# Kernel tuning notes

Measured on AMD Instinct MI355X. Metric: run time of the kernel, lower is better.

The kernel has to match this reference:

```python
import jax, jax.numpy as jnp
import numpy as np

B, S, D, H = 2, 2048, 512, 8
E = D // H  # per-head depth = 64


def setup_inputs() -> dict:
    key = jax.random.key(0)
    ks = jax.random.split(key, 10)
    x = jax.random.normal(ks[0], (B, S, D), dtype=jnp.float32)
    # binary mask: 1 = masked position (added as -1e9)
    attention_mask = jax.random.randint(ks[1], (B, S, S), 0, 2, dtype=jnp.int32)
    # per-head Dense weights stacked: [H, D, E] (Keras Dense: y = x @ W + b)
    sc = 1.0 / np.sqrt(D)
    Wq = jax.random.normal(ks[2], (H, D, E), dtype=jnp.float32) * sc
    Wk = jax.random.normal(ks[3], (H, D, E), dtype=jnp.float32) * sc
    Wv = jax.random.normal(ks[4], (H, D, E), dtype=jnp.float32) * sc
    bq = jnp.zeros((H, E), dtype=jnp.float32)
    bk = jnp.zeros((H, E), dtype=jnp.float32)
    bv = jnp.zeros((H, E), dtype=jnp.float32)
    Wo = jax.random.normal(ks[5], (D, D), dtype=jnp.float32) * sc
    bo = jnp.zeros((D,), dtype=jnp.float32)
    return {"x": x, "attention_mask": attention_mask, "Wq": Wq, "bq": bq,
            "Wk": Wk, "bk": bk, "Wv": Wv, "bv": bv, "Wo": Wo, "bo": bo}


def reference(x, attention_mask, Wq, bq, Wk, bk, Wv, bv, Wo, bo):
    # Per-head Dense projections, vectorized over heads: [B,H,S,E]
    q = jnp.einsum('bsd,hde->bhse', x, Wq) + bq[None, :, None, :]
    k = jnp.einsum('bsd,hde->bhse', x, Wk) + bk[None, :, None, :]
    v = jnp.einsum('bsd,hde->bhse', x, Wv) + bv[None, :, None, :]
    # scaled dot-product attention
    scores = jnp.einsum('bhse,bhte->bhst', q, k) / jnp.sqrt(jnp.float32(E))
    scores = scores + (-1e9) * attention_mask.astype(jnp.float32)[:, None, :, :]
    weights = jax.nn.softmax(scores, axis=-1)
    o = jnp.einsum('bhst,bhte->bhse', weights, v)
    # concat heads (head i -> columns [i*E:(i+1)*E]) then output Dense
    o = o.transpose(0, 2, 1, 3).reshape(B, S, D)
    return o @ Wo + bo
```

## Files before the change

### kernel.cpp

```cpp
#include <hip/hip_runtime.h>
#include <hip/hip_bf16.h>

typedef unsigned short u16;
typedef unsigned int u32;
typedef unsigned long long u64;
typedef short s16x8 __attribute__((ext_vector_type(8)));
typedef float f32x4 __attribute__((ext_vector_type(4)));
typedef float f32x16 __attribute__((ext_vector_type(16)));
typedef int i32x4 __attribute__((ext_vector_type(4)));

static __device__ __forceinline__ u16 f2b(float f) {
    union { float f; unsigned u; } x; x.f = f;
    unsigned r = x.u + 0x7fffu + ((x.u >> 16) & 1u);
    return (u16)(r >> 16);
}

static __device__ __forceinline__ u32 pkbf2(float a, float b) {
    union { __hip_bfloat162 h; u32 u; } c;
    c.h = __float22bfloat162_rn(make_float2(a, b));
    return c.u;
}

static __device__ __forceinline__ f32x16 zero16() {
    f32x16 z;
#pragma unroll
    for (int i = 0; i < 16; i++) z[i] = 0.f;
    return z;
}

static __device__ __forceinline__ s16x8 mk8(u32 a, u32 b, u32 c, u32 d) {
    union { u32 u[4]; s16x8 v; } x;
    x.u[0] = a; x.u[1] = b; x.u[2] = c; x.u[3] = d;
    return x.v;
}

static __device__ __forceinline__ u32 sx32(u32 v) {
    return (u32)__shfl_xor((int)v, 32, 64);
}

static __device__ __forceinline__ void gll16(const u16* g, u16* l) {
    __builtin_amdgcn_global_load_lds(
        (const __attribute__((address_space(1))) u32*)g,
        (__attribute__((address_space(3))) u32*)l, 16, 0, 0);
}


__global__ __launch_bounds__(256)
void k_pack_all(const float* __restrict__ x, const int* __restrict__ mask,
                const float* __restrict__ Wq, const float* __restrict__ Wk,
                const float* __restrict__ Wv, const float* __restrict__ Wo,
                const float* __restrict__ bq, const float* __restrict__ bk,
                const float* __restrict__ bv, const float* __restrict__ bo,
                u16* __restrict__ xb, u16* __restrict__ WT, u16* __restrict__ WoT,
                float* __restrict__ bias, u32* __restrict__ mb) {
    int idx = blockIdx.x * 256 + threadIdx.x;
    if (idx < 524288) {
        int i = idx * 4;
        float4 v = *(const float4*)(x + i);
        ushort4 o;
        o.x = f2b(v.x); o.y = f2b(v.y); o.z = f2b(v.z); o.w = f2b(v.w);
        *(ushort4*)(xb + i) = o;
    } else if (idx < 1310720) {
        int t = idx - 524288;
        int z = t >> 18, r = t & 262143;
        const float* W = (z == 0) ? Wq : (z == 1) ? Wk : Wv;
        int n = r >> 9, d = r & 511;
        WT[t] = f2b(W[((n >> 6) * 512 + d) * 64 + (n & 63)]);
    } else if (idx < 1572864) {
        int r = idx - 1310720;
        int n = r >> 9, d = r & 511;
        WoT[r] = f2b(Wo[d * 512 + n]);
    } else if (idx < 1574912) {
        int i = idx - 1572864;
        float v;
        if (i < 512) v = bq[i];
        else if (i < 1024) v = bk[i - 512];
        else if (i < 1536) v = bv[i - 1024];
        else v = bo[i - 1536];
        bias[i] = v;
    } else {
        int i2 = idx - 1574912;
        const int* p = mask + (size_t)i2 * 32;
        unsigned wv2 = 0;
#pragma unroll
        for (int j = 0; j < 32; j += 4) {
            int4 v = *(const int4*)(p + j);
            wv2 |= ((unsigned)(v.x & 1) << j) | ((unsigned)(v.y & 1) << (j + 1)) |
                   ((unsigned)(v.z & 1) << (j + 2)) | ((unsigned)(v.w & 1) << (j + 3));
        }
        mb[i2] = wv2;
    }
}


template<int MF, bool F32OUT>
__global__ __launch_bounds__(256)
void k_gemm(const u16* __restrict__ A, const u16* __restrict__ BTbase,
            const float* __restrict__ biasBase,
            u16* __restrict__ Cb, u16* __restrict__ Vt, float* __restrict__ Cf) {
    const int BM = MF * 32;
    const int nblk = blockIdx.x, mblk = blockIdx.y, z = blockIdx.z;
    const u16* BT = BTbase + (size_t)z * 262144;
    const float* bias = biasBase + z * 512;
    __shared__ __align__(16) u16 As[MF * 32 * 64];
    __shared__ __align__(16) u16 Bs[128 * 64];
    const int tid = threadIdx.x, lane = tid & 63, wv = tid >> 6;
    const int lr = lane & 15, lg = lane >> 4;
    const int wr = (wv >> 1) * (MF * 16), wc = (wv & 1) * 64;
    const u16* Ag = A + (size_t)(mblk * BM) * 512;
    const u16* Bg = BT + (size_t)(nblk * 128) * 512;

    f32x4 acc[MF][4];
#pragma unroll
    for (int i = 0; i < MF; i++)
#pragma unroll
        for (int j = 0; j < 4; j++) acc[i][j] = (f32x4){0.f, 0.f, 0.f, 0.f};

    for (int kt = 0; kt < 8; kt++) {
        __syncthreads();
#pragma unroll
        for (int i = 0; i < MF; i++) {
            int f = i * 256 + tid, r = f >> 3, c = f & 7;
            *(i32x4*)&As[r * 64 + ((c * 8) ^ ((r & 7) << 3))] =
                *(const i32x4*)(Ag + (size_t)r * 512 + kt * 64 + c * 8);
        }
#pragma unroll
        for (int i = 0; i < 4; i++) {
            int f = i * 256 + tid, r = f >> 3, c = f & 7;
            *(i32x4*)&Bs[r * 64 + ((c * 8) ^ ((r & 7) << 3))] =
                *(const i32x4*)(Bg + (size_t)r * 512 + kt * 64 + c * 8);
        }
        __syncthreads();
#pragma unroll
        for (int ks = 0; ks < 2; ks++) {
            s16x8 af[MF], bf[4];
#pragma unroll
            for (int mf = 0; mf < MF; mf++) {
                int r = wr + mf * 16 + lr;
                af[mf] = *(const s16x8*)&As[r * 64 + ((ks * 32 + lg * 8) ^ ((r & 7) << 3))];
            }
#pragma unroll
            for (int nf = 0; nf < 4; nf++) {
                int r = wc + nf * 16 + lr;
                bf[nf] = *(const s16x8*)&Bs[r * 64 + ((ks * 32 + lg * 8) ^ ((r & 7) << 3))];
            }
#pragma unroll
            for (int mf = 0; mf < MF; mf++)
#pragma unroll
                for (int nf = 0; nf < 4; nf++)
                    acc[mf][nf] = __builtin_amdgcn_mfma_f32_16x16x32_bf16(
                        af[mf], bf[nf], acc[mf][nf], 0, 0, 0);
        }
    }
    const float qsc = (!F32OUT && z == 0) ? 0.18033688011112042f : 1.0f;
#pragma unroll
    for (int nf = 0; nf < 4; nf++) {
        int col = nblk * 128 + wc + nf * 16 + lr;
        float bval = bias[col];
#pragma unroll
        for (int mf = 0; mf < MF; mf++) {
            int row0 = mblk * BM + wr + mf * 16 + lg * 4;
            if (F32OUT) {
#pragma unroll
                for (int r = 0; r < 4; r++)
                    Cf[(size_t)(row0 + r) * 512 + col] = acc[mf][nf][r] + bval;
            } else if (z == 2) {
                ushort4 o;
                o.x = f2b(acc[mf][nf][0] + bval);
                o.y = f2b(acc[mf][nf][1] + bval);
                o.z = f2b(acc[mf][nf][2] + bval);
                o.w = f2b(acc[mf][nf][3] + bval);
                *(ushort4*)(Vt + (size_t)(row0 >> 11) * 1048576 +
                            (size_t)col * 2048 + (row0 & 2047)) = o;
            } else {
#pragma unroll
                for (int r = 0; r < 4; r++)
                    Cb[(size_t)z * 2097152 + (size_t)(row0 + r) * 512 + col] =
                        f2b((acc[mf][nf][r] + bval) * qsc);
            }
        }
    }
}


__global__ __launch_bounds__(256, 2)
void k_attn(const u16* __restrict__ qkv, const u16* __restrict__ vt,
            const u32* __restrict__ mb, u16* __restrict__ oc) {
    const int qt = blockIdx.x, h = blockIdx.y, b = blockIdx.z;
    const u16* Qb = qkv + (size_t)b * 1048576 + h * 64;
    const u16* Kb = Qb + 2097152;
    const u16* VtH = vt + (size_t)b * 1048576 + (size_t)h * 131072;

    __shared__ __align__(16) u16 SMEM[32768];
    __shared__ float Lbuf[4][64];

    const int tid = threadIdx.x;
    const int lane = tid & 63, w = tid >> 6;
    const int hi = lane >> 5, l31 = lane & 31;
    const int qrow = qt * 64 + l31;

    s16x8 qfl[4], qfh[4];
#pragma unroll
    for (int ks = 0; ks < 4; ks++) {
        qfl[ks] = *(const s16x8*)(Qb + (size_t)qrow * 512 + ks * 16 + hi * 8);
        qfh[ks] = *(const s16x8*)(Qb + (size_t)(qrow + 32) * 512 + ks * 16 + hi * 8);
    }

    const int lr8 = lane >> 3, lc8 = (lane & 7) ^ lr8;
    const int vr16 = lane >> 2, vc4 = (lane & 3) ^ ((lane >> 3) & 3);
    const int kv0 = w * 512;

    const u16* kptr = Kb + (size_t)(kv0 + lr8) * 512 + lc8 * 8;
    const u16* vptr = VtH + (size_t)vr16 * 2048 + kv0 + vc4 * 8;
    const u32* mbl = mb + (size_t)(b * 2048 + qrow) * 64 + w * 16;
    const u32* mbh = mbl + 2048;

    u16* wbase = &SMEM[w * 8192];

#pragma unroll
    for (int i = 0; i < 4; i++) {
        gll16(kptr + (size_t)(i * 8) * 512, wbase + i * 512);
        gll16(vptr + (size_t)(i * 16) * 2048, wbase + 2048 + i * 512);
    }
    u32 ml = mbl[0], mh = mbh[0];

    f32x16 aL0 = zero16(), aL1 = zero16(), aH0 = zero16(), aH1 = zero16();
    f32x4 lvl = (f32x4){0.f, 0.f, 0.f, 0.f}, lvh = (f32x4){0.f, 0.f, 0.f, 0.f};
    const int kswz = (l31 & 7) << 3;
    const int vkey = (l31 >> 1) & 3;

    for (int t = 0; t < 16; t++) {
        const u16* Kq = wbase + (t & 1) * 4096;
        const u16* Vq = Kq + 2048;
        u32 mnl = 0, mnh = 0;
        if (t < 15) {
            const u16* kp = kptr + (size_t)((t + 1) * 32) * 512;
            const u16* vp = vptr + (t + 1) * 32;
            u16* db = wbase + (((t + 1) & 1) << 12);
#pragma unroll
            for (int i = 0; i < 4; i++) {
                gll16(kp + (size_t)(i * 8) * 512, db + i * 512);
                gll16(vp + (size_t)(i * 16) * 2048, db + 2048 + i * 512);
            }
            mnl = mbl[t + 1];
            mnh = mbh[t + 1];
            asm volatile("s_waitcnt vmcnt(10)" ::: "memory");
        } else {
            asm volatile("s_waitcnt vmcnt(0)" ::: "memory");
        }
        __builtin_amdgcn_sched_barrier(0);

        f32x16 sl = zero16(), sh = zero16();
        __builtin_amdgcn_s_setprio(1);
#pragma unroll
        for (int ks = 0; ks < 4; ks++) {
            s16x8 kf = *(const s16x8*)&Kq[l31 * 64 + ((ks * 16 + hi * 8) ^ kswz)];
            sl = __builtin_amdgcn_mfma_f32_32x32x16_bf16(kf, qfl[ks], sl, 0, 0, 0);
            sh = __builtin_amdgcn_mfma_f32_32x32x16_bf16(kf, qfh[ks], sh, 0, 0, 0);
        }
        __builtin_amdgcn_s_setprio(0);

        s16x8 pal0, pal1, pah0, pah1;
        {
            const u32 mw = ml >> (hi * 4);
            u32 pk[8];
#pragma unroll
            for (int g = 0; g < 8; g++) {
                const int p0 = ((2 * g) & 3) + 8 * (g >> 1);
                float a = ((mw >> p0) & 1u) ? 0.f : __builtin_amdgcn_exp2f(sl[2 * g]);
                float b2 = ((mw >> (p0 + 1)) & 1u) ? 0.f : __builtin_amdgcn_exp2f(sl[2 * g + 1]);
                lvl[(2 * g) & 3] += a;
                lvl[(2 * g + 1) & 3] += b2;
                pk[g] = pkbf2(a, b2);
            }
            u32 xa = sx32(hi ? pk[0] : pk[2]);
            u32 xb = sx32(hi ? pk[1] : pk[3]);
            u32 xc = sx32(hi ? pk[4] : pk[6]);
            u32 xd = sx32(hi ? pk[5] : pk[7]);
            pal0 = hi ? mk8(xa, xb, pk[2], pk[3]) : mk8(pk[0], pk[1], xa, xb);
            pal1 = hi ? mk8(xc, xd, pk[6], pk[7]) : mk8(pk[4], pk[5], xc, xd);
        }
        {
            const u32 mw = mh >> (hi * 4);
            u32 pk[8];
#pragma unroll
            for (int g = 0; g < 8; g++) {
                const int p0 = ((2 * g) & 3) + 8 * (g >> 1);
                float a = ((mw >> p0) & 1u) ? 0.f : __builtin_amdgcn_exp2f(sh[2 * g]);
                float b2 = ((mw >> (p0 + 1)) & 1u) ? 0.f : __builtin_amdgcn_exp2f(sh[2 * g + 1]);
                lvh[(2 * g) & 3] += a;
                lvh[(2 * g + 1) & 3] += b2;
                pk[g] = pkbf2(a, b2);
            }
            u32 xa = sx32(hi ? pk[0] : pk[2]);
            u32 xb = sx32(hi ? pk[1] : pk[3]);
            u32 xc = sx32(hi ? pk[4] : pk[6]);
            u32 xd = sx32(hi ? pk[5] : pk[7]);
            pah0 = hi ? mk8(xa, xb, pk[2], pk[3]) : mk8(pk[0], pk[1], xa, xb);
            pah1 = hi ? mk8(xc, xd, pk[6], pk[7]) : mk8(pk[4], pk[5], xc, xd);
        }

        __builtin_amdgcn_s_setprio(1);
#pragma unroll
        for (int ksg = 0; ksg < 2; ksg++) {
            const int off = ((ksg * 2 + hi) ^ vkey) << 3;
            s16x8 bv0 = *(const s16x8*)&Vq[l31 * 32 + off];
            s16x8 bv1 = *(const s16x8*)&Vq[(32 + l31) * 32 + off];
            s16x8 pl = ksg ? pal1 : pal0;
            s16x8 ph = ksg ? pah1 : pah0;
            aL0 = __builtin_amdgcn_mfma_f32_32x32x16_bf16(pl, bv0, aL0, 0, 0, 0);
            aL1 = __builtin_amdgcn_mfma_f32_32x32x16_bf16(pl, bv1, aL1, 0, 0, 0);
            aH0 = __builtin_amdgcn_mfma_f32_32x32x16_bf16(ph, bv0, aH0, 0, 0, 0);
            aH1 = __builtin_amdgcn_mfma_f32_32x32x16_bf16(ph, bv1, aH1, 0, 0, 0);
        }
        __builtin_amdgcn_s_setprio(0);

        ml = mnl; mh = mnh;
    }

    float Lsl = (lvl[0] + lvl[1]) + (lvl[2] + lvl[3]);
    Lsl += __shfl_xor(Lsl, 32, 64);
    float Lsh = (lvh[0] + lvh[1]) + (lvh[2] + lvh[3]);
    Lsh += __shfl_xor(Lsh, 32, 64);
    if (lane < 32) { Lbuf[w][l31] = Lsl; Lbuf[w][32 + l31] = Lsh; }

    float* Obuf = (float*)SMEM;
    const int lx = (lane & 7) * 4;
    const int ob = w * 4096 + lane * 32;
#pragma unroll
    for (int g = 0; g < 4; g++) {
        *(f32x4*)&Obuf[ob + ((4 * g) ^ lx)] =
            (f32x4){aL0[4 * g], aL0[4 * g + 1], aL0[4 * g + 2], aL0[4 * g + 3]};
        *(f32x4*)&Obuf[ob + ((16 + 4 * g) ^ lx)] =
            (f32x4){aL1[4 * g], aL1[4 * g + 1], aL1[4 * g + 2], aL1[4 * g + 3]};
        *(f32x4*)&Obuf[ob + 2048 + ((4 * g) ^ lx)] =
            (f32x4){aH0[4 * g], aH0[4 * g + 1], aH0[4 * g + 2], aH0[4 * g + 3]};
        *(f32x4*)&Obuf[ob + 2048 + ((16 + 4 * g) ^ lx)] =
            (f32x4){aH1[4 * g], aH1[4 * g + 1], aH1[4 * g + 2], aH1[4 * g + 3]};
    }
    __syncthreads();

    const int qg2 = w & 1, eh = w >> 1;
    const int rb2 = qg2 * 2048 + lane * 32;
#pragma unroll
    for (int g = 0; g < 4; g++) {
        const int off = (16 * eh + 4 * g) ^ lx;
        f32x4 s0 = *(const f32x4*)&Obuf[rb2 + off];
        f32x4 s1 = *(const f32x4*)&Obuf[4096 + rb2 + off];
        f32x4 s2 = *(const f32x4*)&Obuf[8192 + rb2 + off];
        f32x4 s3 = *(const f32x4*)&Obuf[12288 + rb2 + off];
        f32x4 sum = (s0 + s1) + (s2 + s3);
#pragma unroll
        for (int j = 0; j < 4; j++) {
            const int q = j + 4 * hi + 8 * g;
            float D = Lbuf[0][qg2 * 32 + q] + Lbuf[1][qg2 * 32 + q] +
                      Lbuf[2][qg2 * 32 + q] + Lbuf[3][qg2 * 32 + q];
            const size_t orow = ((size_t)b * 2048 + qt * 64 + qg2 * 32 + q) * 512 +
                                h * 64 + eh * 32;
            oc[orow + l31] = f2b(sum[j] / D);
        }
    }
}


extern "C" void kernel_launch(void* const* d_in, const int* in_sizes, int n_in,
                              void* d_out, int out_size, void* d_ws, size_t ws_size,
                              hipStream_t stream) {
    const float* x    = (const float*)d_in[0];
    const int*   mask = (const int*)d_in[1];
    const float* Wq   = (const float*)d_in[2];
    const float* bq   = (const float*)d_in[3];
    const float* Wk   = (const float*)d_in[4];
    const float* bk   = (const float*)d_in[5];
    const float* Wv   = (const float*)d_in[6];
    const float* bv   = (const float*)d_in[7];
    const float* Wo   = (const float*)d_in[8];
    const float* bo   = (const float*)d_in[9];

    u16* xb     = (u16*)d_ws;
    u16* WT     = xb + 2097152;
    u16* WoT    = WT + 786432;
    u16* qkv    = WoT + 262144;
    u16* vtp    = qkv + 4194304;
    u16* oc     = qkv + 6291456;
    float* bias = (float*)(oc + 2097152);
    u32* mbits  = (u32*)(bias + 2048);

    k_pack_all<<<7176, 256, 0, stream>>>(x, mask, Wq, Wk, Wv, Wo, bq, bk, bv, bo,
                                         xb, WT, WoT, bias, mbits);
    k_gemm<2, false><<<dim3(4, 64, 3), 256, 0, stream>>>(xb, WT, bias, qkv, vtp, nullptr);
    k_attn<<<dim3(32, 8, 2), 256, 0, stream>>>(qkv, vtp, mbits, oc);
    k_gemm<2, true><<<dim3(4, 64, 1), 256, 0, stream>>>(oc, WoT, bias + 1536,
                                                        nullptr, nullptr, (float*)d_out);
}
```

Baseline: 80.04 us.

## Single-buffer V tiles and split epilogue to cut LDS for 3 blocks/CU

Shrinks attention shared memory from 64KB to 48KB by single-buffering the V tile, whose next-tile prefetch is now issued after the PV MFMAs of the current tile, while K stays double-buffered. The cross-wave output reduction is split into two passes (low and high 32-row halves), so the float staging buffer fits in the smaller LDS. Launch bounds are raised to 3 blocks per CU to increase occupancy. The trade-off is less latency hiding for V loads, plus extra barriers and LDS round trips in the epilogue.

```diff
diff --git a/kernel.cpp b/kernel.cpp
--- a/kernel.cpp
+++ b/kernel.cpp
@@ -183,7 +183,7 @@
 }
 
 
-__global__ __launch_bounds__(256, 2)
+__global__ __launch_bounds__(256, 3)
 void k_attn(const u16* __restrict__ qkv, const u16* __restrict__ vt,
             const u32* __restrict__ mb, u16* __restrict__ oc) {
     const int qt = blockIdx.x, h = blockIdx.y, b = blockIdx.z;
@@ -191,7 +191,7 @@
     const u16* Kb = Qb + 2097152;
     const u16* VtH = vt + (size_t)b * 1048576 + (size_t)h * 131072;
 
-    __shared__ __align__(16) u16 SMEM[32768];
+    __shared__ __align__(16) u16 SMEM[24576];
     __shared__ float Lbuf[4][64];
 
     const int tid = threadIdx.x;
@@ -215,14 +215,16 @@
     const u32* mbl = mb + (size_t)(b * 2048 + qrow) * 64 + w * 16;
     const u32* mbh = mbl + 2048;
 
-    u16* wbase = &SMEM[w * 8192];
-
-#pragma unroll
-    for (int i = 0; i < 4; i++) {
+    u16* wbase = &SMEM[w * 6144];
+    u16* Vq = wbase + 4096;
+
+#pragma unroll
+    for (int i = 0; i < 4; i++)
         gll16(kptr + (size_t)(i * 8) * 512, wbase + i * 512);
-        gll16(vptr + (size_t)(i * 16) * 2048, wbase + 2048 + i * 512);
-    }
     u32 ml = mbl[0], mh = mbh[0];
+#pragma unroll
+    for (int i = 0; i < 4; i++)
+        gll16(vptr + (size_t)(i * 16) * 2048, Vq + i * 512);
 
     f32x16 aL0 = zero16(), aL1 = zero16(), aH0 = zero16(), aH1 = zero16();
     f32x4 lvl = (f32x4){0.f, 0.f, 0.f, 0.f}, lvh = (f32x4){0.f, 0.f, 0.f, 0.f};
@@ -230,21 +232,17 @@
     const int vkey = (l31 >> 1) & 3;
 
     for (int t = 0; t < 16; t++) {
-        const u16* Kq = wbase + (t & 1) * 4096;
-        const u16* Vq = Kq + 2048;
+        const u16* Kq = wbase + (t & 1) * 2048;
         u32 mnl = 0, mnh = 0;
         if (t < 15) {
             const u16* kp = kptr + (size_t)((t + 1) * 32) * 512;
-            const u16* vp = vptr + (t + 1) * 32;
-            u16* db = wbase + (((t + 1) & 1) << 12);
-#pragma unroll
-            for (int i = 0; i < 4; i++) {
+            u16* db = wbase + (((t + 1) & 1) << 11);
+#pragma unroll
+            for (int i = 0; i < 4; i++)
                 gll16(kp + (size_t)(i * 8) * 512, db + i * 512);
-                gll16(vp + (size_t)(i * 16) * 2048, db + 2048 + i * 512);
-            }
             mnl = mbl[t + 1];
             mnh = mbh[t + 1];
-            asm volatile("s_waitcnt vmcnt(10)" ::: "memory");
+            asm volatile("s_waitcnt vmcnt(6)" ::: "memory");
         } else {
             asm volatile("s_waitcnt vmcnt(0)" ::: "memory");
         }
@@ -314,7 +312,14 @@
             aH1 = __builtin_amdgcn_mfma_f32_32x32x16_bf16(ph, bv1, aH1, 0, 0, 0);
         }
         __builtin_amdgcn_s_setprio(0);
-
+        __builtin_amdgcn_sched_barrier(0);
+
+        if (t < 15) {
+            const u16* vp = vptr + (t + 1) * 32;
+#pragma unroll
+            for (int i = 0; i < 4; i++)
+                gll16(vp + (size_t)(i * 16) * 2048, Vq + i * 512);
+        }
         ml = mnl; mh = mnh;
     }
 
@@ -326,37 +331,59 @@
 
     float* Obuf = (float*)SMEM;
     const int lx = (lane & 7) * 4;
-    const int ob = w * 4096 + lane * 32;
+    const int ob = w * 2048 + lane * 32;
+    const int eh = w & 1, gg = w >> 1;
+    __syncthreads();
+
 #pragma unroll
     for (int g = 0; g < 4; g++) {
         *(f32x4*)&Obuf[ob + ((4 * g) ^ lx)] =
             (f32x4){aL0[4 * g], aL0[4 * g + 1], aL0[4 * g + 2], aL0[4 * g + 3]};
         *(f32x4*)&Obuf[ob + ((16 + 4 * g) ^ lx)] =
             (f32x4){aL1[4 * g], aL1[4 * g + 1], aL1[4 * g + 2], aL1[4 * g + 3]};
-        *(f32x4*)&Obuf[ob + 2048 + ((4 * g) ^ lx)] =
-            (f32x4){aH0[4 * g], aH0[4 * g + 1], aH0[4 * g + 2], aH0[4 * g + 3]};
-        *(f32x4*)&Obuf[ob + 2048 + ((16 + 4 * g) ^ lx)] =
-            (f32x4){aH1[4 * g], aH1[4 * g + 1], aH1[4 * g + 2], aH1[4 * g + 3]};
     }
     __syncthreads();
-
-    const int qg2 = w & 1, eh = w >> 1;
-    const int rb2 = qg2 * 2048 + lane * 32;
-#pragma unroll
-    for (int g = 0; g < 4; g++) {
+#pragma unroll
+    for (int gi = 0; gi < 2; gi++) {
+        const int g = gg * 2 + gi;
         const int off = (16 * eh + 4 * g) ^ lx;
-        f32x4 s0 = *(const f32x4*)&Obuf[rb2 + off];
-        f32x4 s1 = *(const f32x4*)&Obuf[4096 + rb2 + off];
-        f32x4 s2 = *(const f32x4*)&Obuf[8192 + rb2 + off];
-        f32x4 s3 = *(const f32x4*)&Obuf[12288 + rb2 + off];
+        f32x4 s0 = *(const f32x4*)&Obuf[lane * 32 + off];
+        f32x4 s1 = *(const f32x4*)&Obuf[2048 + lane * 32 + off];
+        f32x4 s2 = *(const f32x4*)&Obuf[4096 + lane * 32 + off];
+        f32x4 s3 = *(const f32x4*)&Obuf[6144 + lane * 32 + off];
         f32x4 sum = (s0 + s1) + (s2 + s3);
 #pragma unroll
         for (int j = 0; j < 4; j++) {
             const int q = j + 4 * hi + 8 * g;
-            float D = Lbuf[0][qg2 * 32 + q] + Lbuf[1][qg2 * 32 + q] +
-                      Lbuf[2][qg2 * 32 + q] + Lbuf[3][qg2 * 32 + q];
-            const size_t orow = ((size_t)b * 2048 + qt * 64 + qg2 * 32 + q) * 512 +
-                                h * 64 + eh * 32;
+            float D = Lbuf[0][q] + Lbuf[1][q] + Lbuf[2][q] + Lbuf[3][q];
+            const size_t orow = ((size_t)b * 2048 + qt * 64 + q) * 512 + h * 64 + eh * 32;
+            oc[orow + l31] = f2b(sum[j] / D);
+        }
+    }
+    __syncthreads();
+
+#pragma unroll
+    for (int g = 0; g < 4; g++) {
+        *(f32x4*)&Obuf[ob + ((4 * g) ^ lx)] =
+            (f32x4){aH0[4 * g], aH0[4 * g + 1], aH0[4 * g + 2], aH0[4 * g + 3]};
+        *(f32x4*)&Obuf[ob + ((16 + 4 * g) ^ lx)] =
+            (f32x4){aH1[4 * g], aH1[4 * g + 1], aH1[4 * g + 2], aH1[4 * g + 3]};
+    }
+    __syncthreads();
+#pragma unroll
+    for (int gi = 0; gi < 2; gi++) {
+        const int g = gg * 2 + gi;
+        const int off = (16 * eh + 4 * g) ^ lx;
+        f32x4 s0 = *(const f32x4*)&Obuf[lane * 32 + off];
+        f32x4 s1 = *(const f32x4*)&Obuf[2048 + lane * 32 + off];
+        f32x4 s2 = *(const f32x4*)&Obuf[4096 + lane * 32 + off];
+        f32x4 s3 = *(const f32x4*)&Obuf[6144 + lane * 32 + off];
+        f32x4 sum = (s0 + s1) + (s2 + s3);
+#pragma unroll
+        for (int j = 0; j < 4; j++) {
+            const int q = j + 4 * hi + 8 * g;
+            float D = Lbuf[0][32 + q] + Lbuf[1][32 + q] + Lbuf[2][32 + q] + Lbuf[3][32 + q];
+            const size_t orow = ((size_t)b * 2048 + qt * 64 + 32 + q) * 512 + h * 64 + eh * 32;
             oc[orow + l31] = f2b(sum[j] / D);
         }
     }
```

Result: no change. 80.77 us (+0.9%).
